# Kernel tuning notes

Hardware: AMD Instinct MI355X
Metric: run time of the kernel (lower is better)

## Reference

```python
import jax, jax.numpy as jnp
import numpy as np

DIM = 768
HEADS = 12
HEAD_DIM = DIM // HEADS
HIDDEN = 4 * DIM


def layernorm(x, g, b, eps=1e-5):
    mu = jnp.mean(x, axis=-1, keepdims=True)
    var = jnp.var(x, axis=-1, keepdims=True)
    return (x - mu) * jax.lax.rsqrt(var + eps) * g + b


def setup_inputs() -> dict:
    key = jax.random.key(0)
    ks = jax.random.split(key, 12)
    s_qkv = 1.0 / np.sqrt(DIM)
    s_h = 1.0 / np.sqrt(HIDDEN)
    return {
        "x": jax.random.normal(ks[0], (8, 1024, DIM), dtype=jnp.float32),
        "ln1_g": jnp.ones((DIM,), jnp.float32),
        "ln1_b": jnp.zeros((DIM,), jnp.float32),
        "w_qkv": jax.random.normal(ks[1], (DIM, 3 * DIM), jnp.float32) * s_qkv,
        "b_qkv": jnp.zeros((3 * DIM,), jnp.float32),
        "w_proj": jax.random.normal(ks[2], (DIM, DIM), jnp.float32) * s_qkv,
        "b_proj": jnp.zeros((DIM,), jnp.float32),
        "ln2_g": jnp.ones((DIM,), jnp.float32),
        "ln2_b": jnp.zeros((DIM,), jnp.float32),
        "w_fc1": jax.random.normal(ks[3], (DIM, HIDDEN), jnp.float32) * s_qkv,
        "b_fc1": jnp.zeros((HIDDEN,), jnp.float32),
        "w_fc2": jax.random.normal(ks[4], (HIDDEN, DIM), jnp.float32) * s_h,
        "b_fc2": jnp.zeros((DIM,), jnp.float32),
    }


def reference(x, ln1_g, ln1_b, w_qkv, b_qkv, w_proj, b_proj,
              ln2_g, ln2_b, w_fc1, b_fc1, w_fc2, b_fc2):
    B, N, C = x.shape
    scale = HEAD_DIM ** -0.5
    # --- attention branch (pre-LN) ---
    h = layernorm(x, ln1_g, ln1_b)
    qkv = h @ w_qkv + b_qkv                      # [B,N,3C]
    qkv = qkv.reshape(B, N, 3, HEADS, HEAD_DIM).transpose(2, 0, 3, 1, 4)
    q, k, v = qkv[0], qkv[1], qkv[2]             # [B,H,N,D]
    attn = jnp.einsum("bhqd,bhkd->bhqk", q, k) * scale
    attn = jnp.clip(attn, -50.0, 50.0)
    attn = jax.nn.softmax(attn, axis=-1)
    o = jnp.einsum("bhqk,bhkd->bhqd", attn, v)   # [B,H,N,D]
    o = o.transpose(0, 2, 1, 3).reshape(B, N, C)
    x = x + (o @ w_proj + b_proj)
    # --- MLP branch (pre-LN) ---
    h = layernorm(x, ln2_g, ln2_b)
    h = jax.nn.gelu(h @ w_fc1 + b_fc1, approximate=False)
    x = x + (h @ w_fc2 + b_fc2)
    return x
```

## Files before the change

kernel.cpp:

```cpp
#include <hip/hip_runtime.h>
#include <hip/hip_bf16.h>

typedef __attribute__((ext_vector_type(8))) short short8;
typedef __attribute__((ext_vector_type(4))) float f32x4;
typedef __attribute__((ext_vector_type(4))) unsigned short us4;

#define DIMC 768
#define HIDDENC 3072
#define NTOK 8192
#define SEQ 1024
#define NHEAD 12
#define HDIM 64

__device__ inline unsigned short f2bf(float f) {
  union { float f; unsigned u; } x; x.f = f;
  unsigned r = (x.u + 0x7FFFu + ((x.u >> 16) & 1u)) >> 16;
  return (unsigned short)r;
}

__device__ inline void gload_lds16(const void* g, void* lds) {
  __builtin_amdgcn_global_load_lds((const __attribute__((address_space(1))) unsigned*)g,
                                   (__attribute__((address_space(3))) unsigned*)lds, 16, 0, 0);
}

__device__ inline float gelu_fast(float u) {
  const float c2u = u * (1.5957691216f + 0.0713548162f * u * u);
  return u - u * __builtin_amdgcn_rcpf(__expf(c2u) + 1.0f);
}

__global__ void wtrans(const float* __restrict__ W, unsigned short* __restrict__ Wt,
                       int K, int N) {
  __shared__ float tile[32][33];
  const int bx = blockIdx.x * 32;
  const int by = blockIdx.y * 32;
  const int tx = threadIdx.x, ty = threadIdx.y;
#pragma unroll
  for (int i = 0; i < 32; i += 8) tile[ty + i][tx] = W[(size_t)(by + ty + i) * N + bx + tx];
  __syncthreads();
#pragma unroll
  for (int i = 0; i < 32; i += 8)
    Wt[(size_t)(bx + ty + i) * K + by + tx] = f2bf(tile[tx][ty + i]);
}

__global__ void vtrans(const unsigned short* __restrict__ qkv, unsigned short* __restrict__ vT) {
  __shared__ unsigned short tile[32][33];
  const int bc = blockIdx.x * 32;
  const int bn = blockIdx.y * 32;
  const int b = blockIdx.z;
  const int tx = threadIdx.x, ty = threadIdx.y;
#pragma unroll
  for (int i = 0; i < 32; i += 8)
    tile[ty + i][tx] = qkv[(size_t)(b * SEQ + bn + ty + i) * (3 * DIMC) + 2 * DIMC + bc + tx];
  __syncthreads();
#pragma unroll
  for (int i = 0; i < 32; i += 8)
    vT[(size_t)(b * DIMC + bc + ty + i) * SEQ + bn + tx] = tile[tx][ty + i];
}

__global__ __launch_bounds__(256) void ln_768(const float* __restrict__ x,
                                              const float* __restrict__ g,
                                              const float* __restrict__ b,
                                              unsigned short* __restrict__ out) {
  const int row = blockIdx.x;
  const int t = threadIdx.x;
  const float* xr = x + (size_t)row * DIMC;
  float v0 = xr[t], v1 = xr[t + 256], v2 = xr[t + 512];
  float s = v0 + v1 + v2;
  float ss = v0 * v0 + v1 * v1 + v2 * v2;
#pragma unroll
  for (int m = 1; m < 64; m <<= 1) { s += __shfl_xor(s, m); ss += __shfl_xor(ss, m); }
  __shared__ float red[8];
  const int w = t >> 6, l = t & 63;
  if (l == 0) { red[w] = s; red[4 + w] = ss; }
  __syncthreads();
  s = red[0] + red[1] + red[2] + red[3];
  ss = red[4] + red[5] + red[6] + red[7];
  const float mu = s * (1.0f / 768.0f);
  const float var = ss * (1.0f / 768.0f) - mu * mu;
  const float rstd = rsqrtf(var + 1e-5f);
  out[(size_t)row * DIMC + t]       = f2bf((v0 - mu) * rstd * g[t]       + b[t]);
  out[(size_t)row * DIMC + t + 256] = f2bf((v1 - mu) * rstd * g[t + 256] + b[t + 256]);
  out[(size_t)row * DIMC + t + 512] = f2bf((v2 - mu) * rstd * g[t + 512] + b[t + 512]);
}

template <int GELU, int RES, int OUT_BF16, int QSCALE, int COLMAJ>
__global__ __launch_bounds__(256) void gemm_bt64(const unsigned short* __restrict__ A,
                                                 const unsigned short* __restrict__ Bt,
                                                 const float* __restrict__ bias,
                                                 const float* __restrict__ res,
                                                 float* __restrict__ Cf,
                                                 unsigned short* __restrict__ Cb,
                                                 int M, int N, int K) {
  __shared__ __align__(16) unsigned short As[2][64 * 64];
  __shared__ __align__(16) unsigned short Bs[2][128 * 64];
  const int gx = gridDim.x;
  const int nwg = gx * gridDim.y;
  const int orig = blockIdx.y * gx + blockIdx.x;
  const int cpx = nwg >> 3;
  int bxx, byy;
  if (COLMAJ) {
    const int c = orig & 7, i = orig >> 3;
    const int rpc = cpx / gx;
    byy = c * rpc + i % rpc;
    bxx = i / rpc;
  } else {
    const int wg = (orig & 7) * cpx + (orig >> 3);
    bxx = wg % gx;
    byy = wg / gx;
  }
  const int t = threadIdx.x;
  const int w = t >> 6, l = t & 63;
  const int lr = l & 15, lg = l >> 4;
  const unsigned short* Ag = A + (size_t)byy * 64 * K;
  const unsigned short* Bg = Bt + (size_t)bxx * 128 * K;
  const int srow = t >> 3;
  const int sulog = (t & 7) ^ (srow & 7);
  const size_t sa = (size_t)srow * K + (size_t)sulog * 8;
  f32x4 acc[4][2] = {};

  auto stage = [&](int buf, int k0) {
    gload_lds16(Ag + sa + k0, &As[buf][w * 512]);
    gload_lds16(Ag + sa + (size_t)32 * K + k0, &As[buf][2048 + w * 512]);
    gload_lds16(Bg + sa + k0, &Bs[buf][w * 512]);
    gload_lds16(Bg + sa + (size_t)32 * K + k0, &Bs[buf][2048 + w * 512]);
    gload_lds16(Bg + sa + (size_t)64 * K + k0, &Bs[buf][4096 + w * 512]);
    gload_lds16(Bg + sa + (size_t)96 * K + k0, &Bs[buf][6144 + w * 512]);
  };
  auto compute = [&](int buf) {
#pragma unroll
    for (int kc = 0; kc < 2; kc++) {
      const int ux = ((kc * 4 + lg) ^ (lr & 7)) * 16;
      short8 af[4], bf[2];
#pragma unroll
      for (int i = 0; i < 4; i++)
        af[i] = *(const short8*)((const char*)&As[buf][0] + (size_t)(i * 16 + lr) * 128 + ux);
#pragma unroll
      for (int j = 0; j < 2; j++)
        bf[j] = *(const short8*)((const char*)&Bs[buf][0] +
                                 (size_t)((w * 2 + j) * 16 + lr) * 128 + ux);
#pragma unroll
      for (int i = 0; i < 4; i++)
#pragma unroll
        for (int j = 0; j < 2; j++)
          acc[i][j] = __builtin_amdgcn_mfma_f32_16x16x32_bf16(af[i], bf[j], acc[i][j], 0, 0, 0);
    }
  };

  const int nt = K >> 6;
  stage(0, 0);
  for (int tt = 0; tt < nt; ++tt) {
    if (tt + 1 < nt) {
      stage((tt + 1) & 1, (tt + 1) << 6);
      asm volatile("s_waitcnt vmcnt(6)" ::: "memory");
    } else {
      asm volatile("s_waitcnt vmcnt(0)" ::: "memory");
    }
    __builtin_amdgcn_s_barrier();
    __builtin_amdgcn_sched_barrier(0);
    compute(tt & 1);
    __builtin_amdgcn_sched_barrier(0);
    __builtin_amdgcn_s_barrier();
  }

  const int rbase = byy * 64;
  const int cbase = bxx * 128 + w * 32;
#pragma unroll
  for (int i = 0; i < 4; i++)
#pragma unroll
    for (int j = 0; j < 2; j++) {
      const int c = cbase + j * 16 + lr;
      const float bz = bias[c];
#pragma unroll
      for (int v = 0; v < 4; v++) {
        const int r = rbase + i * 16 + lg * 4 + v;
        float val = acc[i][j][v] + bz;
        if (RES) val += res[(size_t)r * N + c];
        if (GELU) val = gelu_fast(val);
        if (QSCALE) { if (c < DIMC) val *= 0.18033688011112042f; }
        if (OUT_BF16) Cb[(size_t)r * N + c] = f2bf(val);
        else          Cf[(size_t)r * N + c] = val;
      }
    }
}

__global__ __launch_bounds__(256) void attn(const unsigned short* __restrict__ qkv,
                                            const unsigned short* __restrict__ vT,
                                            unsigned short* __restrict__ o) {
  const int orig = blockIdx.x;
  const int b = orig & 7, h = orig >> 7, qt = (orig >> 3) & 15;
  const int t = threadIdx.x, w = t >> 6, l = t & 63;
  const int lr = l & 15, lg = l >> 4;
  const int ld = 3 * DIMC;
  __shared__ __align__(16) unsigned short Ks[128 * 64];
  __shared__ __align__(16) unsigned short Vt[64 * 128];
  __shared__ __align__(16) unsigned short Ps[4][16 * 128];

  const unsigned short* qb = qkv + (size_t)(b * SEQ + qt * 64 + w * 16) * ld + h * HDIM;
  short8 qf0 = *(const short8*)(qb + (size_t)lr * ld + lg * 8);
  short8 qf1 = *(const short8*)(qb + (size_t)lr * ld + 32 + lg * 8);

  const int rk = t >> 1, seg = t & 1;
  const unsigned short* kb_base = qkv + (size_t)(b * SEQ + rk) * ld + DIMC + h * HDIM + seg * 32;
  const int dv = t >> 2, seg4 = t & 3;
  const unsigned short* vrow = vT + (size_t)(b * DIMC + h * HDIM + dv) * SEQ + seg4 * 32;

  short8 ck[4], cv[4];
#pragma unroll
  for (int j = 0; j < 4; j++) ck[j] = *(const short8*)(kb_base + j * 8);
#pragma unroll
  for (int j = 0; j < 4; j++) cv[j] = *(const short8*)(vrow + j * 8);

  float m_run = -1e30f, l_run = 0.f;
  f32x4 oacc[4];
#pragma unroll
  for (int i = 0; i < 4; i++) oacc[i] = (f32x4){0.f, 0.f, 0.f, 0.f};

  for (int kt = 0; kt < 8; ++kt) {
    {
      char* ksb = (char*)Ks + rk * 128;
      const int swk = (rk & 7) << 4;
#pragma unroll
      for (int j = 0; j < 4; j++)
        *(short8*)(ksb + ((seg * 64 + j * 16) ^ swk)) = ck[j];
      char* vsb = (char*)Vt + dv * 256;
      const int swv = (dv & 7) << 4;
#pragma unroll
      for (int j = 0; j < 4; j++)
        *(short8*)(vsb + ((seg4 * 64 + j * 16) ^ swv)) = cv[j];
    }
    const int nk = (kt + 1) & 7;
    short8 nkk[4], nvv[4];
#pragma unroll
    for (int j = 0; j < 4; j++)
      nkk[j] = *(const short8*)(kb_base + (size_t)nk * 128 * ld + j * 8);
#pragma unroll
    for (int j = 0; j < 4; j++)
      nvv[j] = *(const short8*)(vrow + nk * 128 + j * 8);

    asm volatile("s_waitcnt lgkmcnt(0)" ::: "memory");
    __builtin_amdgcn_s_barrier();
    __builtin_amdgcn_sched_barrier(0);

    f32x4 sf[8];
#pragma unroll
    for (int n = 0; n < 8; n++) sf[n] = (f32x4){0.f, 0.f, 0.f, 0.f};
#pragma unroll
    for (int kc = 0; kc < 2; kc++) {
      short8 q = kc ? qf1 : qf0;
#pragma unroll
      for (int n = 0; n < 8; n++) {
        const int row = n * 16 + lr;
        short8 kf = *(const short8*)((const char*)Ks + row * 128 +
                                     (((kc * 32 + lg * 8) * 2) ^ ((row & 7) << 4)));
        sf[n] = __builtin_amdgcn_mfma_f32_16x16x32_bf16(kf, q, sf[n], 0, 0, 0);
      }
    }

    float tmax = -1e30f;
#pragma unroll
    for (int n = 0; n < 8; n++)
#pragma unroll
      for (int v = 0; v < 4; v++) tmax = fmaxf(tmax, sf[n][v]);
    tmax = fmaxf(tmax, __shfl_xor(tmax, 16));
    tmax = fmaxf(tmax, __shfl_xor(tmax, 32));
    if (!__all(tmax <= m_run + 8.0f)) {
      const float mn = fmaxf(m_run, tmax);
      const float alpha = __builtin_amdgcn_exp2f(m_run - mn);
      m_run = mn;
      l_run *= alpha;
#pragma unroll
      for (int dn = 0; dn < 4; dn++)
#pragma unroll
        for (int v = 0; v < 4; v++) oacc[dn][v] *= alpha;
    }
    float psum = 0.f;
    char* psw = (char*)&Ps[w][0] + lr * 256;
    const int psx = (lr & 7) << 4;
#pragma unroll
    for (int n = 0; n < 8; n++) {
      const float e0 = __builtin_amdgcn_exp2f(sf[n][0] - m_run);
      const float e1 = __builtin_amdgcn_exp2f(sf[n][1] - m_run);
      const float e2 = __builtin_amdgcn_exp2f(sf[n][2] - m_run);
      const float e3 = __builtin_amdgcn_exp2f(sf[n][3] - m_run);
      psum += (e0 + e1) + (e2 + e3);
      unsigned p01, p23;
      asm("v_cvt_pk_bf16_f32 %0, %1, %2" : "=v"(p01) : "v"(e0), "v"(e1));
      asm("v_cvt_pk_bf16_f32 %0, %1, %2" : "=v"(p23) : "v"(e2), "v"(e3));
      const unsigned long long pk = ((unsigned long long)p23 << 32) | p01;
      *(unsigned long long*)(psw + ((n * 32 + lg * 8) ^ psx)) = pk;
    }
    psum += __shfl_xor(psum, 16);
    psum += __shfl_xor(psum, 32);
    l_run += psum;

    asm volatile("s_waitcnt lgkmcnt(0)" ::: "memory");
    __builtin_amdgcn_sched_barrier(0);

#pragma unroll
    for (int kc2 = 0; kc2 < 4; kc2++) {
      short8 pf = *(const short8*)((const char*)&Ps[w][0] + lr * 256 +
                                   (((kc2 * 32 + lg * 8) * 2) ^ ((lr & 7) << 4)));
#pragma unroll
      for (int dn = 0; dn < 4; dn++) {
        const int row = dn * 16 + lr;
        short8 vf = *(const short8*)((const char*)Vt + row * 256 +
                                     (((kc2 * 32 + lg * 8) * 2) ^ ((row & 7) << 4)));
        oacc[dn] = __builtin_amdgcn_mfma_f32_16x16x32_bf16(vf, pf, oacc[dn], 0, 0, 0);
      }
    }
    __builtin_amdgcn_sched_barrier(0);
    __builtin_amdgcn_s_barrier();
#pragma unroll
    for (int j = 0; j < 4; j++) { ck[j] = nkk[j]; cv[j] = nvv[j]; }
  }

  unsigned short* ob = o + (size_t)(b * SEQ + qt * 64 + w * 16 + lr) * DIMC + h * HDIM;
  const float inv = 1.0f / l_run;
#pragma unroll
  for (int dn = 0; dn < 4; dn++) {
    us4 pk;
#pragma unroll
    for (int v = 0; v < 4; v++) pk[v] = f2bf(oacc[dn][v] * inv);
    *(us4*)(ob + dn * 16 + lg * 4) = pk;
  }
}

extern "C" void kernel_launch(void* const* d_in, const int* in_sizes, int n_in,
                              void* d_out, int out_size, void* d_ws, size_t ws_size,
                              hipStream_t stream) {
  const float* x      = (const float*)d_in[0];
  const float* ln1_g  = (const float*)d_in[1];
  const float* ln1_b  = (const float*)d_in[2];
  const float* w_qkv  = (const float*)d_in[3];
  const float* b_qkv  = (const float*)d_in[4];
  const float* w_proj = (const float*)d_in[5];
  const float* b_proj = (const float*)d_in[6];
  const float* ln2_g  = (const float*)d_in[7];
  const float* ln2_b  = (const float*)d_in[8];
  const float* w_fc1  = (const float*)d_in[9];
  const float* b_fc1  = (const float*)d_in[10];
  const float* w_fc2  = (const float*)d_in[11];
  const float* b_fc2  = (const float*)d_in[12];
  float* out = (float*)d_out;

  char* p = (char*)d_ws;
  unsigned short* wqkvT  = (unsigned short*)p; p += (size_t)2304 * 768 * 2;
  unsigned short* wprojT = (unsigned short*)p; p += (size_t)768 * 768 * 2;
  unsigned short* wfc1T  = (unsigned short*)p; p += (size_t)3072 * 768 * 2;
  unsigned short* wfc2T  = (unsigned short*)p; p += (size_t)768 * 3072 * 2;
  unsigned short* h1     = (unsigned short*)p; p += (size_t)NTOK * 768 * 2;
  float*          x1     = (float*)p;          p += (size_t)NTOK * 768 * 4;
  unsigned short* qkv    = (unsigned short*)p; p += (size_t)NTOK * 2304 * 2;
  unsigned short* ob     = (unsigned short*)p; p += (size_t)NTOK * 768 * 2;
  unsigned short* g      = qkv;
  unsigned short* vT     = (unsigned short*)x1;

  dim3 tb(32, 8);
  wtrans<<<dim3(2304 / 32, 768 / 32), tb, 0, stream>>>(w_qkv, wqkvT, 768, 2304);
  wtrans<<<dim3(768 / 32, 768 / 32), tb, 0, stream>>>(w_proj, wprojT, 768, 768);
  wtrans<<<dim3(3072 / 32, 768 / 32), tb, 0, stream>>>(w_fc1, wfc1T, 768, 3072);
  wtrans<<<dim3(768 / 32, 3072 / 32), tb, 0, stream>>>(w_fc2, wfc2T, 3072, 768);

  ln_768<<<NTOK, 256, 0, stream>>>(x, ln1_g, ln1_b, h1);
  gemm_bt64<0, 0, 1, 1, 1><<<dim3(18, 128), 256, 0, stream>>>(h1, wqkvT, b_qkv, nullptr,
                                                              nullptr, qkv, NTOK, 2304, 768);
  vtrans<<<dim3(24, 32, 8), tb, 0, stream>>>(qkv, vT);
  attn<<<dim3(1536), 256, 0, stream>>>(qkv, vT, ob);
  gemm_bt64<0, 1, 0, 0, 1><<<dim3(6, 128), 256, 0, stream>>>(ob, wprojT, b_proj, x, x1,
                                                             nullptr, NTOK, 768, 768);
  ln_768<<<NTOK, 256, 0, stream>>>(x1, ln2_g, ln2_b, h1);
  gemm_bt64<1, 0, 1, 0, 1><<<dim3(24, 128), 256, 0, stream>>>(h1, wfc1T, b_fc1, nullptr,
                                                              nullptr, g, NTOK, 3072, 768);
  gemm_bt64<0, 1, 0, 0, 0><<<dim3(6, 128), 256, 0, stream>>>(g, wfc2T, b_fc2, x1, out,
                                                             nullptr, NTOK, 768, 3072);
}
```

Baseline: 256.6 us.

## Fuse V transpose into QKV GEMM epilogue and merge weight transposes

The QKV GEMM epilogue now writes the V slice directly in transposed [B,C,N] bf16 layout, which removes the separate vtrans kernel and its extra read/write of V. The four weight-transpose launches are merged into one kernel that dispatches on block index. This is meant to save launch overhead and memory traffic, at the cost of narrower, strided 8-byte stores in the V epilogue.

```diff
diff --git a/kernel.cpp b/kernel.cpp
--- a/kernel.cpp
+++ b/kernel.cpp
@@ -28,11 +28,18 @@
   return u - u * __builtin_amdgcn_rcpf(__expf(c2u) + 1.0f);
 }
 
-__global__ void wtrans(const float* __restrict__ W, unsigned short* __restrict__ Wt,
-                       int K, int N) {
+__global__ void wtrans4(const float* __restrict__ w0, const float* __restrict__ w1,
+                        const float* __restrict__ w2, const float* __restrict__ w3,
+                        unsigned short* __restrict__ o0, unsigned short* __restrict__ o1,
+                        unsigned short* __restrict__ o2, unsigned short* __restrict__ o3) {
+  int id = blockIdx.x;
+  const float* W; unsigned short* Wt; int K, N, bxi, byi;
+  if (id < 1728)      {             W = w0; Wt = o0; K = 768;  N = 2304; bxi = id % 72; byi = id / 72; }
+  else if (id < 2304) { id -= 1728; W = w1; Wt = o1; K = 768;  N = 768;  bxi = id % 24; byi = id / 24; }
+  else if (id < 4608) { id -= 2304; W = w2; Wt = o2; K = 768;  N = 3072; bxi = id % 96; byi = id / 96; }
+  else                { id -= 4608; W = w3; Wt = o3; K = 3072; N = 768;  bxi = id % 24; byi = id / 24; }
   __shared__ float tile[32][33];
-  const int bx = blockIdx.x * 32;
-  const int by = blockIdx.y * 32;
+  const int bx = bxi * 32, by = byi * 32;
   const int tx = threadIdx.x, ty = threadIdx.y;
 #pragma unroll
   for (int i = 0; i < 32; i += 8) tile[ty + i][tx] = W[(size_t)(by + ty + i) * N + bx + tx];
@@ -40,21 +47,6 @@
 #pragma unroll
   for (int i = 0; i < 32; i += 8)
     Wt[(size_t)(bx + ty + i) * K + by + tx] = f2bf(tile[tx][ty + i]);
-}
-
-__global__ void vtrans(const unsigned short* __restrict__ qkv, unsigned short* __restrict__ vT) {
-  __shared__ unsigned short tile[32][33];
-  const int bc = blockIdx.x * 32;
-  const int bn = blockIdx.y * 32;
-  const int b = blockIdx.z;
-  const int tx = threadIdx.x, ty = threadIdx.y;
-#pragma unroll
-  for (int i = 0; i < 32; i += 8)
-    tile[ty + i][tx] = qkv[(size_t)(b * SEQ + bn + ty + i) * (3 * DIMC) + 2 * DIMC + bc + tx];
-  __syncthreads();
-#pragma unroll
-  for (int i = 0; i < 32; i += 8)
-    vT[(size_t)(b * DIMC + bc + ty + i) * SEQ + bn + tx] = tile[tx][ty + i];
 }
 
 __global__ __launch_bounds__(256) void ln_768(const float* __restrict__ x,
@@ -83,13 +75,14 @@
   out[(size_t)row * DIMC + t + 512] = f2bf((v2 - mu) * rstd * g[t + 512] + b[t + 512]);
 }
 
-template <int GELU, int RES, int OUT_BF16, int QSCALE, int COLMAJ>
+template <int GELU, int RES, int OUT_BF16, int QSCALE, int COLMAJ, int VTOUT>
 __global__ __launch_bounds__(256) void gemm_bt64(const unsigned short* __restrict__ A,
                                                  const unsigned short* __restrict__ Bt,
                                                  const float* __restrict__ bias,
                                                  const float* __restrict__ res,
                                                  float* __restrict__ Cf,
                                                  unsigned short* __restrict__ Cb,
+                                                 unsigned short* __restrict__ Vout,
                                                  int M, int N, int K) {
   __shared__ __align__(16) unsigned short As[2][64 * 64];
   __shared__ __align__(16) unsigned short Bs[2][128 * 64];
@@ -164,6 +157,23 @@
 
   const int rbase = byy * 64;
   const int cbase = bxx * 128 + w * 32;
+  if (VTOUT && cbase >= 2 * DIMC) {
+#pragma unroll
+    for (int i = 0; i < 4; i++) {
+      const int r0 = rbase + i * 16 + lg * 4;
+      const int bb = r0 >> 10, n = r0 & 1023;
+#pragma unroll
+      for (int j = 0; j < 2; j++) {
+        const int c = cbase + j * 16 + lr;
+        const float bz = bias[c];
+        us4 pk;
+#pragma unroll
+        for (int v = 0; v < 4; v++) pk[v] = f2bf(acc[i][j][v] + bz);
+        *(us4*)(Vout + ((size_t)(bb * DIMC + (c - 2 * DIMC)) << 10) + n) = pk;
+      }
+    }
+    return;
+  }
 #pragma unroll
   for (int i = 0; i < 4; i++)
 #pragma unroll
@@ -355,22 +365,17 @@
   unsigned short* g      = qkv;
   unsigned short* vT     = (unsigned short*)x1;
 
-  dim3 tb(32, 8);
-  wtrans<<<dim3(2304 / 32, 768 / 32), tb, 0, stream>>>(w_qkv, wqkvT, 768, 2304);
-  wtrans<<<dim3(768 / 32, 768 / 32), tb, 0, stream>>>(w_proj, wprojT, 768, 768);
-  wtrans<<<dim3(3072 / 32, 768 / 32), tb, 0, stream>>>(w_fc1, wfc1T, 768, 3072);
-  wtrans<<<dim3(768 / 32, 3072 / 32), tb, 0, stream>>>(w_fc2, wfc2T, 3072, 768);
-
+  wtrans4<<<dim3(6912), dim3(32, 8), 0, stream>>>(w_qkv, w_proj, w_fc1, w_fc2,
+                                                  wqkvT, wprojT, wfc1T, wfc2T);
   ln_768<<<NTOK, 256, 0, stream>>>(x, ln1_g, ln1_b, h1);
-  gemm_bt64<0, 0, 1, 1, 1><<<dim3(18, 128), 256, 0, stream>>>(h1, wqkvT, b_qkv, nullptr,
-                                                              nullptr, qkv, NTOK, 2304, 768);
-  vtrans<<<dim3(24, 32, 8), tb, 0, stream>>>(qkv, vT);
+  gemm_bt64<0, 0, 1, 1, 1, 1><<<dim3(18, 128), 256, 0, stream>>>(
+      h1, wqkvT, b_qkv, nullptr, nullptr, qkv, vT, NTOK, 2304, 768);
   attn<<<dim3(1536), 256, 0, stream>>>(qkv, vT, ob);
-  gemm_bt64<0, 1, 0, 0, 1><<<dim3(6, 128), 256, 0, stream>>>(ob, wprojT, b_proj, x, x1,
-                                                             nullptr, NTOK, 768, 768);
+  gemm_bt64<0, 1, 0, 0, 1, 0><<<dim3(6, 128), 256, 0, stream>>>(
+      ob, wprojT, b_proj, x, x1, nullptr, nullptr, NTOK, 768, 768);
   ln_768<<<NTOK, 256, 0, stream>>>(x1, ln2_g, ln2_b, h1);
-  gemm_bt64<1, 0, 1, 0, 1><<<dim3(24, 128), 256, 0, stream>>>(h1, wfc1T, b_fc1, nullptr,
-                                                              nullptr, g, NTOK, 3072, 768);
-  gemm_bt64<0, 1, 0, 0, 0><<<dim3(6, 128), 256, 0, stream>>>(g, wfc2T, b_fc2, x1, out,
-                                                             nullptr, NTOK, 768, 3072);
-}
+  gemm_bt64<1, 0, 1, 0, 1, 0><<<dim3(24, 128), 256, 0, stream>>>(
+      h1, wfc1T, b_fc1, nullptr, nullptr, g, nullptr, NTOK, 3072, 768);
+  gemm_bt64<0, 1, 0, 0, 0, 0><<<dim3(6, 128), 256, 0, stream>>>(
+      g, wfc2T, b_fc2, x1, out, nullptr, nullptr, NTOK, 768, 3072);
+}
```

Result: faster. 247.4 us (-3.6%).
